# Optimization experiments

Measured on AMD Instinct MI355X. Metric: run time of the kernel, lower is better.

The kernel has to match this reference:

```python
import jax, jax.numpy as jnp
import numpy as np

N_LAYERS = 2          # number of (Dense, Erf) pairs before final Dense
PI = np.float32(np.pi)
EPS = np.float32(1e-7)


def setup_inputs() -> dict:
    key = jax.random.key(0)
    kx, ky = jax.random.split(key)
    x = jax.random.normal(kx, (8192, 512), dtype=jnp.float32)
    y = jax.random.normal(ky, (8192, 512), dtype=jnp.float32)
    return {"x": x, "y": y}


def _erf_diag(c):
    # E[erf(u)^2] for u ~ N(0, c):  (2/pi) * arcsin(2c / (1 + 2c))
    return (2.0 / PI) * jnp.arcsin(2.0 * c / (1.0 + 2.0 * c))


def reference(x, y):
    d = x.shape[1]
    inv_d = jnp.float32(1.0 / d)
    # First Dense (W_std=1, no bias): nngp = x.y^T / d, ntk = nngp
    nngp = (x @ y.T) * inv_d                      # [n, m]
    cx = jnp.sum(x * x, axis=1) * inv_d           # [n] diagonal second moments
    cy = jnp.sum(y * y, axis=1) * inv_d           # [m]
    ntk = nngp
    for _ in range(N_LAYERS):
        # Erf nonlinearity (analytic arcsine kernel)
        prod = (1.0 + 2.0 * cx)[:, None] * (1.0 + 2.0 * cy)[None, :]  # [n, m]
        ratio = jnp.clip(2.0 * nngp * jax.lax.rsqrt(prod), -1.0 + EPS, 1.0 - EPS)
        nngp_new = (2.0 / PI) * jnp.arcsin(ratio)
        dot = (4.0 / PI) * jax.lax.rsqrt(jnp.maximum(prod - 4.0 * nngp * nngp, EPS))
        ntk = ntk * dot
        nngp = nngp_new
        cx = _erf_diag(cx)
        cy = _erf_diag(cy)
        # Dense (W_std=1, no bias): nngp unchanged, ntk += nngp
        ntk = ntk + nngp
    return ntk  # kernel_type == 'ntk'
```

## Files before the change

### kernel.cpp

```cpp
#include <hip/hip_runtime.h>
#include <hip/hip_bf16.h>
#include <math.h>

#define D_K  512
#define NROW 8192
#define BM   128
#define BN   128
#define BK   64

typedef __attribute__((ext_vector_type(8))) short bf16x8;
typedef __attribute__((ext_vector_type(4))) float f32x4;

#if __has_builtin(__builtin_amdgcn_rsqf)
#define RSQ(x) __builtin_amdgcn_rsqf(x)
#else
#define RSQ(x) rsqrtf(x)
#endif

__device__ __forceinline__ unsigned short f2bf(float f) {
    unsigned int u = __float_as_uint(f);
    unsigned int r = (u + 0x7FFFu + ((u >> 16) & 1u)) >> 16;
    return (unsigned short)r;
}

__device__ __forceinline__ void load_lds16(const unsigned short* g, unsigned short* l) {
    __builtin_amdgcn_global_load_lds(
        (const __attribute__((address_space(1))) unsigned int*)g,
        (__attribute__((address_space(3))) unsigned int*)l,
        16, 0, 0);
}

__global__ void prep_kernel(const float* __restrict__ xin, const float* __restrict__ yin,
                            unsigned short* __restrict__ xb, unsigned short* __restrict__ yb,
                            float* __restrict__ px0, float* __restrict__ px1,
                            float* __restrict__ py0, float* __restrict__ py1)
{
    const int row   = blockIdx.x;
    const int which = blockIdx.y;
    const float* src = (which ? yin : xin) + (size_t)row * D_K;
    unsigned short* dst = (which ? yb : xb) + (size_t)row * D_K;
    const int t = threadIdx.x;

    float2 v = ((const float2*)src)[t];
    ushort2 b; b.x = f2bf(v.x); b.y = f2bf(v.y);
    ((ushort2*)dst)[t] = b;

    float s = v.x * v.x + v.y * v.y;
    for (int o = 32; o > 0; o >>= 1) s += __shfl_down(s, o, 64);
    __shared__ float red[4];
    if ((t & 63) == 0) red[t >> 6] = s;
    __syncthreads();
    if (t == 0) {
        float tot = red[0] + red[1] + red[2] + red[3];
        float c0 = tot * (1.0f / D_K);
        float a0 = 1.0f + 2.0f * c0;
        float c1 = 0.636619772367581343f * asinf(2.0f * c0 / a0);
        float a1 = 1.0f + 2.0f * c1;
        if (which) {
            py0[row] = 1.0f / sqrtf(a0);
            py1[row] = 1.0f / sqrtf(a1);
        } else {
            px0[row] = 2.0f / sqrtf(a0);
            px1[row] = 2.0f / sqrtf(a1);
        }
    }
}

__device__ __forceinline__ void layer_step(float& nngp, float& ntk, float s) {
    float ratio = nngp * s;
    ratio = fminf(fmaxf(ratio, -0.9999999f), 0.9999999f);
    float u = ratio * ratio;
    float p = fmaf(u, 0.011046346f, 0.014241648f);
    p = fmaf(u, p, 0.019340246f);
    p = fmaf(u, p, 0.028420525f);
    p = fmaf(u, p, 0.047746483f);
    p = fmaf(u, p, 0.106103295f);
    p = fmaf(u, p, 0.636619772f);
    float nngp_new = ratio * p;
    float rv = RSQ(1.0f - u);
    float dot = 0.636619772f * (s * rv);
    ntk = fmaf(ntk, dot, nngp_new);
    nngp = nngp_new;
}

__global__ void ntk_kernel(const unsigned short* __restrict__ xb,
                           const unsigned short* __restrict__ yb,
                           const float* __restrict__ px0, const float* __restrict__ px1,
                           const float* __restrict__ py0, const float* __restrict__ py1,
                           float* __restrict__ out)
{
    __shared__ unsigned short As[BM * BK];
    __shared__ unsigned short Bs[BN * BK];

    const int tid  = threadIdx.x;
    const int lane = tid & 63;
    const int wid  = tid >> 6;
    const int wr   = wid >> 1;
    const int wc   = wid & 1;
    const int rowBase = blockIdx.y * BM;
    const int colBase = blockIdx.x * BN;
    const int l15 = lane & 15;
    const int lg  = lane >> 4;

    f32x4 acc[4][4];
    #pragma unroll
    for (int m = 0; m < 4; m++)
        #pragma unroll
        for (int n = 0; n < 4; n++)
            acc[m][n] = (f32x4){0.f, 0.f, 0.f, 0.f};

    for (int ks = 0; ks < D_K; ks += BK) {
        __syncthreads();
        #pragma unroll
        for (int r = 0; r < 4; r++) {
            int base = r * 256 + wid * 64;
            int idx  = base + lane;
            int row  = idx >> 3;
            int c    = (idx & 7) ^ (row & 7);
            const unsigned short* gA = xb + (size_t)(rowBase + row) * D_K + ks + c * 8;
            load_lds16(gA, &As[base * 8]);
            const unsigned short* gB = yb + (size_t)(colBase + row) * D_K + ks + c * 8;
            load_lds16(gB, &Bs[base * 8]);
        }
        __syncthreads();

        bf16x8 af[2][4], bfr[2][4];
        #pragma unroll
        for (int s = 0; s < 2; s++) {
            #pragma unroll
            for (int m = 0; m < 4; m++) {
                int rowA = wr * 64 + m * 16 + l15;
                int slA  = ((s * 4 + lg) ^ (rowA & 7)) * 8;
                af[s][m] = *(const bf16x8*)&As[rowA * BK + slA];
                int rowB = wc * 64 + m * 16 + l15;
                int slB  = ((s * 4 + lg) ^ (rowB & 7)) * 8;
                bfr[s][m] = *(const bf16x8*)&Bs[rowB * BK + slB];
            }
        }
        #pragma unroll
        for (int s = 0; s < 2; s++)
            #pragma unroll
            for (int m = 0; m < 4; m++)
                #pragma unroll
                for (int n = 0; n < 4; n++)
                    acc[m][n] = __builtin_amdgcn_mfma_f32_16x16x32_bf16(
                        af[s][m], bfr[s][n], acc[m][n], 0, 0, 0);
    }

    float py0v[4], py1v[4];
    int   colv[4];
    #pragma unroll
    for (int n = 0; n < 4; n++) {
        int col = colBase + wc * 64 + n * 16 + l15;
        colv[n] = col;
        py0v[n] = py0[col];
        py1v[n] = py1[col];
    }
    #pragma unroll
    for (int m = 0; m < 4; m++) {
        int row0 = rowBase + wr * 64 + m * 16 + lg * 4;
        #pragma unroll
        for (int j = 0; j < 4; j++) {
            int row = row0 + j;
            float a0 = px0[row], a1 = px1[row];
            #pragma unroll
            for (int n = 0; n < 4; n++) {
                float nngp = acc[m][n][j] * (1.0f / D_K);
                float ntk = nngp;
                layer_step(nngp, ntk, a0 * py0v[n]);
                layer_step(nngp, ntk, a1 * py1v[n]);
                out[(size_t)row * NROW + colv[n]] = ntk;
            }
        }
    }
}

extern "C" void kernel_launch(void* const* d_in, const int* in_sizes, int n_in,
                              void* d_out, int out_size, void* d_ws, size_t ws_size,
                              hipStream_t stream)
{
    const float* x = (const float*)d_in[0];
    const float* y = (const float*)d_in[1];
    float* out = (float*)d_out;

    char* ws = (char*)d_ws;
    unsigned short* xb = (unsigned short*)ws;
    unsigned short* yb = (unsigned short*)(ws + (size_t)8 * 1024 * 1024);
    float* px0 = (float*)(ws + (size_t)16 * 1024 * 1024);
    float* px1 = px0 + NROW;
    float* py0 = px1 + NROW;
    float* py1 = py0 + NROW;

    dim3 pgrid(NROW, 2);
    prep_kernel<<<pgrid, 256, 0, stream>>>(x, y, xb, yb, px0, px1, py0, py1);

    dim3 grid(NROW / BN, NROW / BM);
    ntk_kernel<<<grid, 256, 0, stream>>>(xb, yb, px0, px1, py0, py1, out);
}
```

Before: 136.2 us.

## Truncate arcsin polynomial, remap blocks per XCD, use nontemporal output stores

The epilogue arcsin polynomial drops from seven to four coefficients, and the 2/pi scale on the derivative term is folded into per-column constants computed once per thread. Blocks are launched on a 1D grid and remapped so that each XCD handles a contiguous band of row tiles, which is meant to improve L2 reuse of the shared A/B panels. Output writes become nontemporal stores so the 256 MB result does not pollute the cache. The shorter polynomial loses accuracy for ratios near ±1, which can reach tolerance limits.

```diff
diff --git a/kernel.cpp b/kernel.cpp
--- a/kernel.cpp
+++ b/kernel.cpp
@@ -66,21 +66,17 @@
     }
 }
 
-__device__ __forceinline__ void layer_step(float& nngp, float& ntk, float s) {
-    float ratio = nngp * s;
-    ratio = fminf(fmaxf(ratio, -0.9999999f), 0.9999999f);
-    float u = ratio * ratio;
-    float p = fmaf(u, 0.011046346f, 0.014241648f);
-    p = fmaf(u, p, 0.019340246f);
-    p = fmaf(u, p, 0.028420525f);
-    p = fmaf(u, p, 0.047746483f);
+__device__ __forceinline__ void layer_step(float& nngp, float& ntk, float s, float sC) {
+    float r = nngp * s;
+    r = fminf(fmaxf(r, -0.9999999f), 0.9999999f);
+    float u = r * r;
+    float p = fmaf(u, 0.028420525f, 0.047746483f);
     p = fmaf(u, p, 0.106103295f);
     p = fmaf(u, p, 0.636619772f);
-    float nngp_new = ratio * p;
+    float nn = r * p;
     float rv = RSQ(1.0f - u);
-    float dot = 0.636619772f * (s * rv);
-    ntk = fmaf(ntk, dot, nngp_new);
-    nngp = nngp_new;
+    ntk = fmaf(ntk, sC * rv, nn);
+    nngp = nn;
 }
 
 __global__ void ntk_kernel(const unsigned short* __restrict__ xb,
@@ -97,8 +93,14 @@
     const int wid  = tid >> 6;
     const int wr   = wid >> 1;
     const int wc   = wid & 1;
-    const int rowBase = blockIdx.y * BM;
-    const int colBase = blockIdx.x * BN;
+
+    const int bid = blockIdx.x;
+    const int xcd = bid & 7;
+    const int idx = bid >> 3;
+    const int by  = xcd * 8 + (idx & 7);
+    const int bx  = idx >> 3;
+    const int rowBase = by * BM;
+    const int colBase = bx * BN;
     const int l15 = lane & 15;
     const int lg  = lane >> 4;
 
@@ -114,9 +116,9 @@
         #pragma unroll
         for (int r = 0; r < 4; r++) {
             int base = r * 256 + wid * 64;
-            int idx  = base + lane;
-            int row  = idx >> 3;
-            int c    = (idx & 7) ^ (row & 7);
+            int cidx = base + lane;
+            int row  = cidx >> 3;
+            int c    = (cidx & 7) ^ (row & 7);
             const unsigned short* gA = xb + (size_t)(rowBase + row) * D_K + ks + c * 8;
             load_lds16(gA, &As[base * 8]);
             const unsigned short* gB = yb + (size_t)(colBase + row) * D_K + ks + c * 8;
@@ -147,7 +149,7 @@
                         af[s][m], bfr[s][n], acc[m][n], 0, 0, 0);
     }
 
-    float py0v[4], py1v[4];
+    float py0v[4], py1v[4], py0C[4], py1C[4];
     int   colv[4];
     #pragma unroll
     for (int n = 0; n < 4; n++) {
@@ -155,6 +157,8 @@
         colv[n] = col;
         py0v[n] = py0[col];
         py1v[n] = py1[col];
+        py0C[n] = 0.636619772f * py0v[n];
+        py1C[n] = 0.636619772f * py1v[n];
     }
     #pragma unroll
     for (int m = 0; m < 4; m++) {
@@ -167,9 +171,9 @@
             for (int n = 0; n < 4; n++) {
                 float nngp = acc[m][n][j] * (1.0f / D_K);
                 float ntk = nngp;
-                layer_step(nngp, ntk, a0 * py0v[n]);
-                layer_step(nngp, ntk, a1 * py1v[n]);
-                out[(size_t)row * NROW + colv[n]] = ntk;
+                layer_step(nngp, ntk, a0 * py0v[n], a0 * py0C[n]);
+                layer_step(nngp, ntk, a1 * py1v[n], a1 * py1C[n]);
+                __builtin_nontemporal_store(ntk, &out[(size_t)row * NROW + colv[n]]);
             }
         }
     }
@@ -194,6 +198,5 @@
     dim3 pgrid(NROW, 2);
     prep_kernel<<<pgrid, 256, 0, stream>>>(x, y, xb, yb, px0, px1, py0, py1);
 
-    dim3 grid(NROW / BN, NROW / BM);
-    ntk_kernel<<<grid, 256, 0, stream>>>(xb, yb, px0, px1, py0, py1, out);
-}
+    ntk_kernel<<<(NROW / BM) * (NROW / BN), 256, 0, stream>>>(xb, yb, px0, px1, py0, py1, out);
+}
```

Measured after the change: 133.4 us. 1.02x faster.
